# Performance work log

Hardware: AMD Instinct MI355X
Metric: run time of the kernel (lower is better)

The kernel has to match this reference:

```python
import jax, jax.numpy as jnp
import numpy as np

B, T, C, U = 16, 128, 64, 128
ODE_UNFOLDS = 6
EPS = 1e-8


def setup_inputs() -> dict:
    key = jax.random.key(0)
    ks = jax.random.split(key, 12)
    u = lambda k, s, lo, hi: jax.random.uniform(k, s, jnp.float32, lo, hi)
    return dict(
        x=jax.random.normal(ks[0], (B, T, C), jnp.float32),
        h0=jnp.zeros((B, U), jnp.float32),
        gleak=u(ks[1], (U,), 0.001, 1.0),
        vleak=u(ks[2], (U,), -0.2, 0.2),
        cm=u(ks[3], (U,), 0.4, 0.6),
        sigma=u(ks[4], (U, U), 3.0, 8.0),
        mu=u(ks[5], (U, U), 0.3, 0.8),
        w=u(ks[6], (U, U), 0.001, 1.0),
        erev=jnp.sign(jax.random.normal(ks[7], (U, U))).astype(jnp.float32),
        sensory_sigma=u(ks[8], (C, U), 3.0, 8.0),
        sensory_mu=u(ks[9], (C, U), 0.3, 0.8),
        sensory_w=u(ks[10], (C, U), 0.001, 1.0),
        sensory_erev=jnp.sign(jax.random.normal(ks[11], (C, U))).astype(jnp.float32),
        input_w=jnp.ones((C,), jnp.float32),
        input_b=jnp.zeros((C,), jnp.float32),
        output_w=jnp.ones((U,), jnp.float32),
        output_b=jnp.zeros((U,), jnp.float32),
    )


def reference(x, h0, gleak, vleak, cm, sigma, mu, w, erev,
              sensory_sigma, sensory_mu, sensory_w, sensory_erev,
              input_w, input_b, output_w, output_b):
    sp = jax.nn.softplus
    # Positive-constrained params (implicit_param_constraints=True)
    w_pos = sp(w)                      # [U,U]
    sw_pos = sp(sensory_w)             # [C,U]
    gl = sp(gleak)                     # [U]
    # elapsed_time ts = 1.0 -> cm_t = softplus(cm) / (1/ode_unfolds)
    cm_t = sp(cm) * ODE_UNFOLDS        # [U]

    def step(h, xt):
        # input affine mapping
        xt = xt * input_w + input_b                                        # [B,C]
        # sensory synapses (constant across unfolds)
        sens_act = sw_pos * jax.nn.sigmoid(sensory_sigma * (xt[:, :, None] - sensory_mu))  # [B,C,U]
        w_num_s = jnp.sum(sens_act * sensory_erev, axis=1)                 # [B,U]
        w_den_s = jnp.sum(sens_act, axis=1)                                # [B,U]
        v = h
        for _ in range(ODE_UNFOLDS):
            # recurrent synapses: pre dim 1, post dim 2
            w_act = w_pos * jax.nn.sigmoid(sigma * (v[:, :, None] - mu))   # [B,U,U]
            w_num = jnp.sum(w_act * erev, axis=1) + w_num_s                # [B,U]
            w_den = jnp.sum(w_act, axis=1) + w_den_s                       # [B,U]
            num = cm_t * v + gl * vleak + w_num
            den = cm_t + gl + w_den
            v = num / (den + EPS)
        out = v * output_w + output_b   # motor_size == units for FullyConnected
        return v, out

    h_final, outs = jax.lax.scan(step, h0, jnp.swapaxes(x, 0, 1))  # outs: [T,B,U]
    readout = jnp.swapaxes(outs, 0, 1)                             # [B,T,U]
    return readout, h_final
```

## Files before the change

kernel.cpp:

```cpp
#include <hip/hip_runtime.h>

#define NB 16
#define NT 128
#define NC 64
#define NU 128
#define UNFOLDS 6
#define LTC_EPS 1e-8f
#define LOG2E 1.44269504088896340736f

__global__ __launch_bounds__(512, 2)
void ltc_kernel(const float* __restrict__ x,
                const float* __restrict__ h0,
                const float* __restrict__ gleak,
                const float* __restrict__ vleak,
                const float* __restrict__ cm,
                const float* __restrict__ sigma,
                const float* __restrict__ mu,
                const float* __restrict__ w,
                const float* __restrict__ erev,
                const float* __restrict__ ssigma,
                const float* __restrict__ smu,
                const float* __restrict__ sw,
                const float* __restrict__ serev,
                const float* __restrict__ iw,
                const float* __restrict__ ib,
                const float* __restrict__ ow,
                const float* __restrict__ ob,
                float* __restrict__ out)
{
    __shared__ __align__(16) float xt_all[NT * NC];
    __shared__ __align__(16) float v_lds[NU];
    __shared__ __align__(16) float2 red[512];
    __shared__ __align__(16) float2 red_s[512];

    const int tid = threadIdx.x;
    const int b   = blockIdx.x;
    const int j   = tid & (NU - 1);
    const int k   = tid >> 7;

    float rA[32], rB[32], rW[32];
#pragma unroll
    for (int c = 0; c < 32; ++c) {
        int i = k * 32 + c;
        float sg = sigma[i * NU + j];
        float m  = mu[i * NU + j];
        float wp = log1pf(expf(w[i * NU + j]));
        float er = erev[i * NU + j];
        float a  = -sg * LOG2E;
        rA[c] = a;
        rB[c] = -a * m;
        rW[c] = wp * er;
    }
    float sA[16], sB[16], sWr[16];
#pragma unroll
    for (int c = 0; c < 16; ++c) {
        int i = k * 16 + c;
        float sg = ssigma[i * NU + j];
        float m  = smu[i * NU + j];
        float wp = log1pf(expf(sw[i * NU + j]));
        float er = serev[i * NU + j];
        float a  = -sg * LOG2E;
        sA[c]  = a;
        sB[c]  = -a * m;
        sWr[c] = wp * er;
    }

    float cmt = 0.f, gl = 0.f, glv = 0.f, owj = 0.f, obj = 0.f, vj = 0.f;
    if (tid < NU) {
        cmt = 6.0f * log1pf(expf(cm[tid]));
        gl  = log1pf(expf(gleak[tid]));
        glv = gl * vleak[tid];
        owj = ow[tid];
        obj = ob[tid];
        vj  = h0[b * NU + tid];
        v_lds[tid] = vj;
    }

#pragma unroll
    for (int r = 0; r < (NT * NC) / 512; ++r) {
        int idx = r * 512 + tid;
        int c   = idx & (NC - 1);
        xt_all[idx] = x[b * NT * NC + idx] * iw[c] + ib[c];
    }
    __syncthreads();

    for (int t = 0; t < NT; ++t) {
        {
            const float* xt = &xt_all[t * NC + k * 16];
            float np0 = 0.f, np1 = 0.f, dp0 = 0.f, dp1 = 0.f;
#pragma unroll
            for (int c = 0; c < 16; ++c) {
                float tt = fmaf(sA[c], xt[c], sB[c]);
                float e  = __builtin_amdgcn_exp2f(tt);
                float r  = __builtin_amdgcn_rcpf(1.0f + e);
                if (c & 1) { np1 = fmaf(sWr[c], r, np1); dp1 = fmaf(fabsf(sWr[c]), r, dp1); }
                else       { np0 = fmaf(sWr[c], r, np0); dp0 = fmaf(fabsf(sWr[c]), r, dp0); }
            }
            red_s[tid] = make_float2(np0 + np1, dp0 + dp1);
        }
        __syncthreads();
        float snum = 0.f, sden = 0.f;
        if (tid < NU) {
            float2 p0 = red_s[tid],          p1 = red_s[NU + tid];
            float2 p2 = red_s[2 * NU + tid], p3 = red_s[3 * NU + tid];
            snum = (p0.x + p1.x) + (p2.x + p3.x);
            sden = (p0.y + p1.y) + (p2.y + p3.y);
        }

        for (int u = 0; u < UNFOLDS; ++u) {
            float vi[32];
#pragma unroll
            for (int q = 0; q < 8; ++q) {
                float4 vv = *(const float4*)&v_lds[k * 32 + q * 4];
                vi[q * 4 + 0] = vv.x; vi[q * 4 + 1] = vv.y;
                vi[q * 4 + 2] = vv.z; vi[q * 4 + 3] = vv.w;
            }
            float np0 = 0.f, np1 = 0.f, dp0 = 0.f, dp1 = 0.f;
#pragma unroll
            for (int c = 0; c < 32; ++c) {
                float tt = fmaf(rA[c], vi[c], rB[c]);
                float e  = __builtin_amdgcn_exp2f(tt);
                float r  = __builtin_amdgcn_rcpf(1.0f + e);
                if (c & 1) { np1 = fmaf(rW[c], r, np1); dp1 = fmaf(fabsf(rW[c]), r, dp1); }
                else       { np0 = fmaf(rW[c], r, np0); dp0 = fmaf(fabsf(rW[c]), r, dp0); }
            }
            red[tid] = make_float2(np0 + np1, dp0 + dp1);
            __syncthreads();
            if (tid < NU) {
                float2 p0 = red[tid],          p1 = red[NU + tid];
                float2 p2 = red[2 * NU + tid], p3 = red[3 * NU + tid];
                float wn = (p0.x + p1.x) + (p2.x + p3.x) + snum;
                float wd = (p0.y + p1.y) + (p2.y + p3.y) + sden;
                float numf = fmaf(cmt, vj, glv) + wn;
                float denf = cmt + gl + wd + LTC_EPS;
                vj = numf / denf;
                v_lds[tid] = vj;
            }
            __syncthreads();
        }

        if (tid < NU) {
            out[(b * NT + t) * NU + tid] = fmaf(vj, owj, obj);
        }
    }
    if (tid < NU) {
        out[NB * NT * NU + b * NU + tid] = vj;
    }
}

extern "C" void kernel_launch(void* const* d_in, const int* in_sizes, int n_in,
                              void* d_out, int out_size, void* d_ws, size_t ws_size,
                              hipStream_t stream) {
    const float* x      = (const float*)d_in[0];
    const float* h0     = (const float*)d_in[1];
    const float* gleak  = (const float*)d_in[2];
    const float* vleak  = (const float*)d_in[3];
    const float* cm     = (const float*)d_in[4];
    const float* sigma  = (const float*)d_in[5];
    const float* mu     = (const float*)d_in[6];
    const float* w      = (const float*)d_in[7];
    const float* erev   = (const float*)d_in[8];
    const float* ssig   = (const float*)d_in[9];
    const float* smu    = (const float*)d_in[10];
    const float* sw     = (const float*)d_in[11];
    const float* serev  = (const float*)d_in[12];
    const float* iw     = (const float*)d_in[13];
    const float* ibv    = (const float*)d_in[14];
    const float* ow     = (const float*)d_in[15];
    const float* ob     = (const float*)d_in[16];
    float* out = (float*)d_out;

    ltc_kernel<<<NB, 512, 0, stream>>>(x, h0, gleak, vleak, cm, sigma, mu, w, erev,
                                       ssig, smu, sw, serev, iw, ibv, ow, ob, out);
}
```

Measured before the change: 869.5 us.

## Precompute sensory terms in parallel kernel and use quad DPP reductions with one barrier

Moves the sensory-synapse reduction, which does not depend on the recurrent state, into a separate fully parallel kernel over all (batch, time) pairs and writes the results to workspace. The sequential kernel prefetches those values one step ahead. It also remaps threads so that the four partial sums for each unit sit in one quad, reduces them with DPP lane permutes instead of LDS, and double-buffers v so each unfold needs one barrier instead of two. The cost is an extra launch, workspace traffic, and every thread now doing the per-unit update redundantly.

```diff
diff --git a/kernel.cpp b/kernel.cpp
--- a/kernel.cpp
+++ b/kernel.cpp
@@ -7,145 +7,192 @@
 #define UNFOLDS 6
 #define LTC_EPS 1e-8f
 #define LOG2E 1.44269504088896340736f
-
+#define LN2   0.69314718055994530942f
+
+__device__ __forceinline__ float fast_softplus(float x) {
+    return LN2 * __builtin_amdgcn_logf(1.0f + __builtin_amdgcn_exp2f(x * LOG2E));
+}
+
+template<int CTRL>
+__device__ __forceinline__ float qperm(float x) {
+    return __int_as_float(__builtin_amdgcn_update_dpp(
+        0, __float_as_int(x), CTRL, 0xF, 0xF, true));
+}
+__device__ __forceinline__ float quad_sum(float x) {
+    x += qperm<0xB1>(x);
+    x += qperm<0x4E>(x);
+    return x;
+}
+
+__global__ __launch_bounds__(128)
+void ltc_sens_kernel(const float* __restrict__ x,
+                     const float* __restrict__ ssigma,
+                     const float* __restrict__ smu,
+                     const float* __restrict__ sw,
+                     const float* __restrict__ serev,
+                     const float* __restrict__ iw,
+                     const float* __restrict__ ib,
+                     float2* __restrict__ sens)
+{
+    __shared__ float xt[NC];
+    const int blk = blockIdx.x;
+    const int b = blk >> 7;
+    const int t = blk & (NT - 1);
+    const int j = threadIdx.x;
+    if (j < NC) xt[j] = fmaf(x[(b * NT + t) * NC + j], iw[j], ib[j]);
+    __syncthreads();
+
+    float n0 = 0.f, n1 = 0.f, d0 = 0.f, d1 = 0.f;
+#pragma unroll 8
+    for (int c = 0; c < NC; ++c) {
+        const int idx = c * NU + j;
+        float sg = ssigma[idx];
+        float m  = smu[idx];
+        float wp = fast_softplus(sw[idx]);
+        float er = serev[idx];
+        float tt = (m - xt[c]) * (sg * LOG2E);
+        float e  = __builtin_amdgcn_exp2f(tt);
+        float r  = __builtin_amdgcn_rcpf(1.0f + e);
+        float wr = wp * r;
+        if (c & 1) { n1 = fmaf(wr, er, n1); d1 += wr; }
+        else       { n0 = fmaf(wr, er, n0); d0 += wr; }
+    }
+    sens[(b * NT + t) * NU + j] = make_float2(n0 + n1, d0 + d1);
+}
+
+template<bool USE_WS>
 __global__ __launch_bounds__(512, 2)
-void ltc_kernel(const float* __restrict__ x,
-                const float* __restrict__ h0,
-                const float* __restrict__ gleak,
-                const float* __restrict__ vleak,
-                const float* __restrict__ cm,
-                const float* __restrict__ sigma,
-                const float* __restrict__ mu,
-                const float* __restrict__ w,
-                const float* __restrict__ erev,
-                const float* __restrict__ ssigma,
-                const float* __restrict__ smu,
-                const float* __restrict__ sw,
-                const float* __restrict__ serev,
-                const float* __restrict__ iw,
-                const float* __restrict__ ib,
-                const float* __restrict__ ow,
-                const float* __restrict__ ob,
-                float* __restrict__ out)
+void ltc_seq_kernel(const float* __restrict__ x,
+                    const float* __restrict__ h0,
+                    const float* __restrict__ gleak,
+                    const float* __restrict__ vleak,
+                    const float* __restrict__ cm,
+                    const float* __restrict__ sigma,
+                    const float* __restrict__ mu,
+                    const float* __restrict__ w,
+                    const float* __restrict__ erev,
+                    const float* __restrict__ ssigma,
+                    const float* __restrict__ smu,
+                    const float* __restrict__ sw,
+                    const float* __restrict__ serev,
+                    const float* __restrict__ iw,
+                    const float* __restrict__ ibv,
+                    const float* __restrict__ ow,
+                    const float* __restrict__ ob,
+                    const float2* __restrict__ sens,
+                    float* __restrict__ out)
 {
-    __shared__ __align__(16) float xt_all[NT * NC];
-    __shared__ __align__(16) float v_lds[NU];
-    __shared__ __align__(16) float2 red[512];
-    __shared__ __align__(16) float2 red_s[512];
+    __shared__ __align__(16) float v_lds[2][NU];
+    __shared__ __align__(16) float xt_all[USE_WS ? 4 : NT * NC];
 
     const int tid = threadIdx.x;
     const int b   = blockIdx.x;
-    const int j   = tid & (NU - 1);
-    const int k   = tid >> 7;
+    const int j   = tid >> 2;
+    const int k   = tid & 3;
 
     float rA[32], rB[32], rW[32];
 #pragma unroll
     for (int c = 0; c < 32; ++c) {
-        int i = k * 32 + c;
-        float sg = sigma[i * NU + j];
-        float m  = mu[i * NU + j];
-        float wp = log1pf(expf(w[i * NU + j]));
-        float er = erev[i * NU + j];
+        const int idx = (k * 32 + c) * NU + j;
+        float sg = sigma[idx];
+        float m  = mu[idx];
+        float wp = fast_softplus(w[idx]);
+        float er = erev[idx];
         float a  = -sg * LOG2E;
         rA[c] = a;
         rB[c] = -a * m;
         rW[c] = wp * er;
     }
+
     float sA[16], sB[16], sWr[16];
-#pragma unroll
-    for (int c = 0; c < 16; ++c) {
-        int i = k * 16 + c;
-        float sg = ssigma[i * NU + j];
-        float m  = smu[i * NU + j];
-        float wp = log1pf(expf(sw[i * NU + j]));
-        float er = serev[i * NU + j];
-        float a  = -sg * LOG2E;
-        sA[c]  = a;
-        sB[c]  = -a * m;
-        sWr[c] = wp * er;
-    }
-
-    float cmt = 0.f, gl = 0.f, glv = 0.f, owj = 0.f, obj = 0.f, vj = 0.f;
-    if (tid < NU) {
-        cmt = 6.0f * log1pf(expf(cm[tid]));
-        gl  = log1pf(expf(gleak[tid]));
-        glv = gl * vleak[tid];
-        owj = ow[tid];
-        obj = ob[tid];
-        vj  = h0[b * NU + tid];
-        v_lds[tid] = vj;
-    }
-
-#pragma unroll
-    for (int r = 0; r < (NT * NC) / 512; ++r) {
-        int idx = r * 512 + tid;
-        int c   = idx & (NC - 1);
-        xt_all[idx] = x[b * NT * NC + idx] * iw[c] + ib[c];
-    }
+    if (!USE_WS) {
+#pragma unroll
+        for (int c = 0; c < 16; ++c) {
+            const int idx = (k * 16 + c) * NU + j;
+            float sg = ssigma[idx];
+            float m  = smu[idx];
+            float wp = fast_softplus(sw[idx]);
+            float er = serev[idx];
+            float a  = -sg * LOG2E;
+            sA[c]  = a;
+            sB[c]  = -a * m;
+            sWr[c] = wp * er;
+        }
+#pragma unroll
+        for (int r = 0; r < (NT * NC) / 512; ++r) {
+            int idx = r * 512 + tid;
+            int cc  = idx & (NC - 1);
+            xt_all[idx] = fmaf(x[b * NT * NC + idx], iw[cc], ibv[cc]);
+        }
+    }
+
+    const float cmt = 6.0f * fast_softplus(cm[j]);
+    const float gl  = fast_softplus(gleak[j]);
+    const float glv = gl * vleak[j];
+    const float owj = ow[j];
+    const float obj = ob[j];
+    float vj = h0[b * NU + j];
+    if (k == 0) v_lds[0][j] = vj;
     __syncthreads();
 
+    int p = 0;
+    float2 s_cur = make_float2(0.f, 0.f);
+    if (USE_WS) s_cur = sens[b * NT * NU + j];
+
     for (int t = 0; t < NT; ++t) {
-        {
+        float snum, sden;
+        float2 s_next = s_cur;
+        if (USE_WS) {
+            snum = s_cur.x; sden = s_cur.y;
+            const int tn = (t + 1 < NT) ? (t + 1) : t;
+            s_next = sens[(b * NT + tn) * NU + j];
+        } else {
             const float* xt = &xt_all[t * NC + k * 16];
-            float np0 = 0.f, np1 = 0.f, dp0 = 0.f, dp1 = 0.f;
+            float n0 = 0.f, n1 = 0.f, d0 = 0.f, d1 = 0.f;
 #pragma unroll
             for (int c = 0; c < 16; ++c) {
                 float tt = fmaf(sA[c], xt[c], sB[c]);
                 float e  = __builtin_amdgcn_exp2f(tt);
                 float r  = __builtin_amdgcn_rcpf(1.0f + e);
-                if (c & 1) { np1 = fmaf(sWr[c], r, np1); dp1 = fmaf(fabsf(sWr[c]), r, dp1); }
-                else       { np0 = fmaf(sWr[c], r, np0); dp0 = fmaf(fabsf(sWr[c]), r, dp0); }
+                if (c & 1) { n1 = fmaf(sWr[c], r, n1); d1 = fmaf(fabsf(sWr[c]), r, d1); }
+                else       { n0 = fmaf(sWr[c], r, n0); d0 = fmaf(fabsf(sWr[c]), r, d0); }
             }
-            red_s[tid] = make_float2(np0 + np1, dp0 + dp1);
-        }
-        __syncthreads();
-        float snum = 0.f, sden = 0.f;
-        if (tid < NU) {
-            float2 p0 = red_s[tid],          p1 = red_s[NU + tid];
-            float2 p2 = red_s[2 * NU + tid], p3 = red_s[3 * NU + tid];
-            snum = (p0.x + p1.x) + (p2.x + p3.x);
-            sden = (p0.y + p1.y) + (p2.y + p3.y);
-        }
-
+            snum = quad_sum(n0 + n1);
+            sden = quad_sum(d0 + d1);
+        }
+
+#pragma unroll
         for (int u = 0; u < UNFOLDS; ++u) {
             float vi[32];
 #pragma unroll
             for (int q = 0; q < 8; ++q) {
-                float4 vv = *(const float4*)&v_lds[k * 32 + q * 4];
+                const float4 vv = *(const float4*)&v_lds[p][k * 32 + q * 4];
                 vi[q * 4 + 0] = vv.x; vi[q * 4 + 1] = vv.y;
                 vi[q * 4 + 2] = vv.z; vi[q * 4 + 3] = vv.w;
             }
-            float np0 = 0.f, np1 = 0.f, dp0 = 0.f, dp1 = 0.f;
+            float n0 = 0.f, n1 = 0.f, d0 = 0.f, d1 = 0.f;
 #pragma unroll
             for (int c = 0; c < 32; ++c) {
                 float tt = fmaf(rA[c], vi[c], rB[c]);
                 float e  = __builtin_amdgcn_exp2f(tt);
                 float r  = __builtin_amdgcn_rcpf(1.0f + e);
-                if (c & 1) { np1 = fmaf(rW[c], r, np1); dp1 = fmaf(fabsf(rW[c]), r, dp1); }
-                else       { np0 = fmaf(rW[c], r, np0); dp0 = fmaf(fabsf(rW[c]), r, dp0); }
+                if (c & 1) { n1 = fmaf(rW[c], r, n1); d1 = fmaf(fabsf(rW[c]), r, d1); }
+                else       { n0 = fmaf(rW[c], r, n0); d0 = fmaf(fabsf(rW[c]), r, d0); }
             }
-            red[tid] = make_float2(np0 + np1, dp0 + dp1);
+            const float wn = quad_sum(n0 + n1) + snum;
+            const float wd = quad_sum(d0 + d1) + sden;
+            const float numf = fmaf(cmt, vj, glv) + wn;
+            const float denf = cmt + gl + wd + LTC_EPS;
+            vj = numf / denf;
+            if (k == 0) v_lds[p ^ 1][j] = vj;
             __syncthreads();
-            if (tid < NU) {
-                float2 p0 = red[tid],          p1 = red[NU + tid];
-                float2 p2 = red[2 * NU + tid], p3 = red[3 * NU + tid];
-                float wn = (p0.x + p1.x) + (p2.x + p3.x) + snum;
-                float wd = (p0.y + p1.y) + (p2.y + p3.y) + sden;
-                float numf = fmaf(cmt, vj, glv) + wn;
-                float denf = cmt + gl + wd + LTC_EPS;
-                vj = numf / denf;
-                v_lds[tid] = vj;
-            }
-            __syncthreads();
-        }
-
-        if (tid < NU) {
-            out[(b * NT + t) * NU + tid] = fmaf(vj, owj, obj);
-        }
-    }
-    if (tid < NU) {
-        out[NB * NT * NU + b * NU + tid] = vj;
-    }
+            p ^= 1;
+        }
+
+        if (k == 0) out[(b * NT + t) * NU + j] = fmaf(vj, owj, obj);
+        s_cur = s_next;
+    }
+    if (k == 0) out[NB * NT * NU + b * NU + j] = vj;
 }
 
 extern "C" void kernel_launch(void* const* d_in, const int* in_sizes, int n_in,
@@ -170,6 +217,16 @@
     const float* ob     = (const float*)d_in[16];
     float* out = (float*)d_out;
 
-    ltc_kernel<<<NB, 512, 0, stream>>>(x, h0, gleak, vleak, cm, sigma, mu, w, erev,
-                                       ssig, smu, sw, serev, iw, ibv, ow, ob, out);
-}
+    const size_t sens_bytes = (size_t)NB * NT * NU * sizeof(float2);
+    if (ws_size >= sens_bytes) {
+        float2* sens = (float2*)d_ws;
+        ltc_sens_kernel<<<NB * NT, 128, 0, stream>>>(x, ssig, smu, sw, serev, iw, ibv, sens);
+        ltc_seq_kernel<true><<<NB, 512, 0, stream>>>(
+            x, h0, gleak, vleak, cm, sigma, mu, w, erev,
+            ssig, smu, sw, serev, iw, ibv, ow, ob, (const float2*)sens, out);
+    } else {
+        ltc_seq_kernel<false><<<NB, 512, 0, stream>>>(
+            x, h0, gleak, vleak, cm, sigma, mu, w, erev,
+            ssig, smu, sw, serev, iw, ibv, ow, ob, nullptr, out);
+    }
+}
```

New measurement: 853.7 us. Within noise of the previous version (-1.8%).
